# Kernel tuning notes

Measured on AMD Instinct MI355X. Metric: run time of the kernel, lower is better.

The kernel has to match this reference:

```python
import jax, jax.numpy as jnp
import numpy as np
from jax import lax

N = 2048


def setup_inputs() -> dict:
    key = jax.random.key(0)
    k1, k2, k3, k4 = jax.random.split(key, 4)
    root_logits = jax.random.normal(k1, (N,), jnp.float32)
    e = jax.random.normal(k2, (N, N), jnp.float32)
    # torch init zeros the diagonal of edge_probs
    edge_logits = e * (1.0 - jnp.eye(N, dtype=jnp.float32))
    # Gumbel noise made explicit so the reference is deterministic
    g_root = jax.random.gumbel(k3, (2, N), jnp.float32)
    g_edge = jax.random.gumbel(k4, (N, 2, N), jnp.float32)
    return {"root_logits": root_logits, "edge_logits": edge_logits,
            "g_root": g_root, "g_edge": g_edge}


def _sample_dag(root_logits, edge_logits, g_root, g_edge):
    n = root_logits.shape[0]
    f32 = jnp.float32
    i32 = jnp.int32

    # --- root sampling: hard gumbel-softmax over {root, not-root}, tau=1 ---
    yr = jnp.stack([jax.nn.log_sigmoid(root_logits),
                    jax.nn.log_sigmoid(-root_logits)]) + g_root  # [2, n]
    soft_r = jax.nn.softmax(yr, axis=0)[0]
    root_bool = yr[0] > yr[1]
    # straight-through: hard forward, soft gradient
    roots = root_bool.astype(f32) + soft_r - lax.stop_gradient(soft_r)

    # --- per-node edge sampling (noise pre-drawn; rows masked by BFS) ---
    ye = jnp.stack([jax.nn.log_sigmoid(edge_logits),
                    jax.nn.log_sigmoid(-edge_logits)], axis=1) + g_edge  # [n,2,n]
    soft_e = jax.nn.softmax(ye, axis=1)[:, 0, :]  # [n, n]
    hard_e = ye[:, 0, :] > ye[:, 1, :]            # [n, n] bool
    st_e = hard_e.astype(f32) + soft_e - lax.stop_gradient(soft_e)

    # --- FIFO queue init with roots in ascending index order ---
    idx = jnp.arange(n, dtype=i32)
    rank = jnp.cumsum(root_bool.astype(i32)) - 1
    pos = jnp.where(root_bool, rank, n)  # slot n is a write-only dump
    queue0 = jnp.zeros(n + 1, i32).at[pos].set(idx, mode='drop')
    tail0 = jnp.sum(root_bool).astype(i32)
    head0 = jnp.int32(0)
    dag0 = jnp.zeros((n, n), f32)
    anc0 = jnp.eye(n, dtype=bool)  # ancestors, anc[i,i]=1
    enq0 = root_bool               # dedup flag (equivalent to torch's pop-skip)

    def step(carry, _):
        dag, anc, queue, enq, head, tail = carry
        active = head < tail
        i = queue[head]
        anc_i = anc[i]  # includes i itself (eye init)
        cand = (1.0 - anc_i.astype(f32)) * (1.0 - roots)
        row = st_e[i] * cand
        dag = dag.at[i].set(jnp.where(active, row, dag[i]))
        children = hard_e[i] & (~anc_i) & (~root_bool) & active
        # anc[j] |= anc[i] | {i} for each child j (anc_i already contains i)
        anc = anc | (children[:, None] & anc_i[None, :])
        new = children & (~enq)
        r = jnp.cumsum(new.astype(i32)) - 1
        p = jnp.where(new, tail + r, n)
        queue = queue.at[p].set(idx, mode='drop')
        enq = enq | new
        tail = tail + jnp.sum(new).astype(i32)
        head = head + active.astype(i32)
        return (dag, anc, queue, enq, head, tail), None

    (dag, _, _, _, _, _), _ = lax.scan(
        step, (dag0, anc0, queue0, enq0, head0, tail0), None, length=n)
    return dag


def reference(root_logits, edge_logits, g_root, g_edge):
    return _sample_dag(root_logits, edge_logits, g_root, g_edge)
```

## Files before the change

kernel.cpp:

```cpp
#include <hip/hip_runtime.h>
#include <stdint.h>

typedef unsigned long long u64;
typedef unsigned int u32;
typedef unsigned short u16;

#define NN 2048
#define NW 32

#if __has_builtin(__builtin_amdgcn_sbfe)
#define SBFE(x, o) ((u32)__builtin_amdgcn_sbfe((int)(x), (u32)(o), 1u))
#else
#define SBFE(x, o) ((u32)(-(int)(((x) >> (o)) & 1u)))
#endif

static __device__ __forceinline__ bool gumbel_gt(float x, float g0, float g1) {
    float L = log1pf(expf(-fabsf(x)));
    float a = (-(fmaxf(-x, 0.f) + L)) + g0;
    float b = (-(fmaxf( x, 0.f) + L)) + g1;
    return a > b;
}

static __device__ __forceinline__ u64 orsel2(u64 acc, u64 w0, u64 w1, u64 m, int b0) {
    u32 mm = (b0 < 32) ? (u32)m : (u32)(m >> 32);
    int sh = b0 & 31;
    u32 s0 = SBFE(mm, sh);
    u32 s1 = SBFE(mm, sh + 1);
    u32 al = (u32)acc | ((u32)w0 & s0) | ((u32)w1 & s1);
    u32 ah = (u32)(acc >> 32) | ((u32)(w0 >> 32) & s0) | ((u32)(w1 >> 32) & s1);
    return ((u64)ah << 32) | al;
}

__global__ __launch_bounds__(256) void prep_kernel(
    const float* __restrict__ edge_logits,
    const float* __restrict__ g_edge,
    u64* __restrict__ heBits)
{
    const int i    = blockIdx.x;
    const int t    = threadIdx.x;
    const int lane = t & 63;
    const int wv   = t >> 6;
    const int j0   = 512 * wv + 8 * lane;

    const float4* xe  = (const float4*)(edge_logits + (size_t)i * NN + j0);
    const float4* ge0 = (const float4*)(g_edge + (size_t)i * (2 * NN) + j0);
    const float4* ge1 = (const float4*)(g_edge + (size_t)i * (2 * NN) + NN + j0);
    float4 xa = xe[0],  xb = xe[1];
    float4 g0a = ge0[0], g0b = ge0[1];
    float4 g1a = ge1[0], g1b = ge1[1];
    float x[8]  = {xa.x, xa.y, xa.z, xa.w, xb.x, xb.y, xb.z, xb.w};
    float g0[8] = {g0a.x, g0a.y, g0a.z, g0a.w, g0b.x, g0b.y, g0b.z, g0b.w};
    float g1[8] = {g1a.x, g1a.y, g1a.z, g1a.w, g1b.x, g1b.y, g1b.z, g1b.w};

    u64 v = 0;
    #pragma unroll
    for (int e = 0; e < 8; ++e)
        v |= (u64)(gumbel_gt(x[e], g0[e], g1[e]) ? 1u : 0u) << e;
    v <<= 8 * (lane & 7);
    v |= __shfl_xor(v, 1);
    v |= __shfl_xor(v, 2);
    v |= __shfl_xor(v, 4);
    if ((lane & 7) == 0)
        heBits[(size_t)i * NW + 8 * wv + (lane >> 3)] = v;
}

static __device__ void order_body(char* smem,
    const float* __restrict__ root_logits, const float* __restrict__ g_root,
    const u64* __restrict__ heBits,
    u16* __restrict__ posr, u16* __restrict__ porderW, int* __restrict__ nrPtr)
{
    int* s_porder = (int*)smem;
    int* s_cnt    = (int*)(smem + 8192);
    u64 (*s_U)[NW]  = (u64(*)[NW])(smem + 16384);
    u64 (*s_Pg)[NW] = (u64(*)[NW])(smem + 20480);
    u16* s_pos = (u16*)(smem + 24576);
    u16* s_f   = (u16*)(smem + 28672);
    u16* s_rk  = (u16*)(smem + 32768);
    u64* s_root = (u64*)(smem + 36864);
    u64* s_enq  = (u64*)(smem + 37120);
    u64* s_F    = (u64*)(smem + 37376);
    int* s_wsum = (int*)(smem + 37632);
    int* s_woff = (int*)(smem + 37696);
    int* s_sc   = (int*)(smem + 37760);
    int &s_base = s_sc[0]; int &s_lo = s_sc[1]; int &s_levcnt = s_sc[2];
    int &s_newcnt = s_sc[3]; int &s_nr = s_sc[4];

    const int t    = threadIdx.x;
    const int lane = t & 63;
    const int wid  = t >> 6;
    const int half = lane >> 5;
    const int w    = lane & 31;

    for (int p = 0; p < 2; ++p) {
        int j = p * 1024 + t;
        bool rb = gumbel_gt(root_logits[j], g_root[j], g_root[NN + j]);
        u64 m = __ballot(rb);
        if (lane == 0) s_root[j >> 6] = m;
    }
    __syncthreads();
    for (int p = 0; p < 2; ++p) {
        int j = p * 1024 + t;
        int ww = j >> 6; u64 bit = 1ull << (j & 63);
        if (s_root[ww] & bit) {
            int r = 0;
            for (int k = 0; k < ww; ++k) r += __popcll(s_root[k]);
            r += __popcll(s_root[ww] & (bit - 1ull));
            s_pos[j] = (u16)r;
            s_porder[r] = j;
        }
    }
    if (t < NW) s_enq[t] = s_root[t];
    if (t == 0) {
        int tl = 0;
        for (int k = 0; k < NW; ++k) tl += __popcll(s_root[k]);
        s_lo = 0; s_levcnt = tl; s_base = tl; s_nr = tl;
    }
    __syncthreads();

    while (s_levcnt > 0 && s_base < NN) {
        const int lo = s_lo, cnt = s_levcnt, base = s_base;
        const int seglen = (cnt + 15) >> 4;
        const int s0 = wid * seglen;
        const int s1 = (s0 + seglen < cnt) ? (s0 + seglen) : cnt;

        {
            u64 acc = 0;
            for (int m = s0 + half; m < s1; m += 2)
                acc |= heBits[(size_t)s_porder[lo + m] * NW + w];
            acc |= __shfl(acc, lane ^ 32);
            if (half == 0) s_U[wid][w] = acc;
        }
        __syncthreads();
        if (t < NW) {
            u64 o = 0;
            #pragma unroll
            for (int s = 0; s < 16; ++s) o |= s_U[s][t];
            s_F[t] = o & ~s_enq[t] & ~s_root[t];
        }
        __syncthreads();
        if (t < 512) {
            int s = t >> 5, ww = t & 31;
            u64 p = 0;
            for (int s2 = 0; s2 < s; ++s2) p |= s_U[s2][ww];
            s_Pg[s][ww] = p & s_F[ww];
        }
        __syncthreads();
        {
            u64 P  = s_Pg[wid][w];
            u64 Fw = s_F[w];
            int myidx = (s0 + lane < s1) ? s_porder[lo + s0 + lane] : 0;
            u64 rnext = 0;
            {
                int rowi0 = __shfl(myidx, half);
                if (s0 + half < s1) rnext = heBits[(size_t)rowi0 * NW + w];
            }
            for (int m = s0; m < s1; m += 2) {
                int m0 = m + half;
                u64 r = rnext;
                {
                    int sidx = (m + 2 - s0) + half;
                    if (sidx > 63) sidx = 0;
                    int rowin = __shfl(myidx, sidx);
                    rnext = 0;
                    if (m + 2 + half < s1) rnext = heBits[(size_t)rowin * NW + w];
                }
                u64 v = (m0 < s1) ? (r & Fw & ~P) : 0ull;
                u64 vlo = __shfl(v, w);
                u64 B = half ? (v & ~vlo) : v;
                int pc = __popcll(B);
                int inc = pc;
                #pragma unroll
                for (int d = 1; d < 32; d <<= 1) {
                    int u2 = __shfl_up(inc, d, 64);
                    if (w >= d) inc += u2;
                }
                int excl = inc - pc;
                int tot = __shfl(inc, (half << 5) | 31);
                if (w == 0 && m0 < s1) s_cnt[m0] = tot;
                u64 mm = B;
                int idx = excl;
                while (mm) {
                    int b = __ffsll(mm) - 1; mm &= mm - 1;
                    int j = (w << 6) + b;
                    s_f[j]  = (u16)m0;
                    s_rk[j] = (u16)idx++;
                }
                P |= B | __shfl(B, lane ^ 32);
            }
        }
        __syncthreads();
        {
            int b0 = 2 * t, b1 = 2 * t + 1;
            int c0 = (b0 < cnt) ? s_cnt[b0] : 0;
            int c1 = (b1 < cnt) ? s_cnt[b1] : 0;
            int pairv = c0 + c1;
            int incl = pairv;
            for (int d = 1; d < 64; d <<= 1) {
                int v = __shfl_up(incl, d, 64);
                if (lane >= d) incl += v;
            }
            if (lane == 63) s_wsum[wid] = incl;
            __syncthreads();
            if (t < 16) {
                int v = s_wsum[t];
                int inc2 = v;
                for (int d = 1; d < 16; d <<= 1) {
                    int u = __shfl_up(inc2, d, 16);
                    if (t >= d) inc2 += u;
                }
                s_woff[t] = inc2 - v;
                if (t == 15) s_newcnt = inc2;
            }
            __syncthreads();
            int excl = s_woff[wid] + (incl - pairv);
            if (b0 < cnt) s_cnt[b0] = excl;
            if (b1 < cnt) s_cnt[b1] = excl + c0;
        }
        __syncthreads();
        for (int p = 0; p < 2; ++p) {
            int j = p * 1024 + t;
            int ww = j >> 6;
            if ((s_F[ww] >> (j & 63)) & 1ull) {
                int slot = base + s_cnt[s_f[j]] + s_rk[j];
                s_pos[j] = (u16)slot;
                s_porder[slot] = j;
            }
        }
        if (t < NW) s_enq[t] |= s_F[t];
        __syncthreads();
        if (t == 0) { s_lo = base; s_levcnt = s_newcnt; s_base = base + s_newcnt; }
        __syncthreads();
    }

    for (int p = 0; p < 2; ++p) {
        int j = p * 1024 + t;
        int ww = j >> 6; u64 bit = 1ull << (j & 63);
        if (!((s_enq[ww] >> (j & 63)) & 1ull)) {
            int rk = 0;
            for (int k2 = 0; k2 < ww; ++k2) rk += __popcll(~s_enq[k2]);
            rk += __popcll(~s_enq[ww] & (bit - 1ull));
            int slot = s_base + rk;
            s_pos[j] = (u16)slot;
            s_porder[slot] = j;
        }
    }
    __syncthreads();
    for (int p = 0; p < 2; ++p) {
        int j = p * 1024 + t;
        int fl = s_pos[j];
        if ((s_root[j >> 6] >> (j & 63)) & 1ull) fl |= 0x8000;
        if ((s_enq[j >> 6]  >> (j & 63)) & 1ull) fl |= 0x4000;
        posr[j] = (u16)fl;
        porderW[j] = (u16)s_porder[j];
    }
    if (t == 0) *nrPtr = s_nr;
}

__global__ __launch_bounds__(1024) void ordtrans_kernel(
    const float* __restrict__ root_logits,
    const float* __restrict__ g_root,
    const u64* __restrict__ heBits,
    u64* __restrict__ heT,
    u16* __restrict__ posr,
    u16* __restrict__ porderW,
    int* __restrict__ nrPtr)
{
    __shared__ __align__(16) char smem[38016];
    const int bid  = blockIdx.x;
    const int t    = threadIdx.x;
    const int lane = t & 63;
    const int wv   = t >> 6;

    if (bid == 0) {
        order_body(smem, root_logits, g_root, heBits, posr, porderW, nrPtr);
    } else {
        int gw = (bid - 1) * 16 + wv;
        if (gw < 1024) {
            int ti = gw >> 5, tj = gw & 31;
            u64 w = heBits[(size_t)(64 * ti + lane) * NW + tj];
            u64 out = 0;
            #pragma unroll
            for (int b = 0; b < 64; ++b) {
                u64 m = __ballot(((w >> b) & 1ull) != 0);
                if (b == lane) out = m;
            }
            heT[(size_t)(64 * tj + lane) * NW + ti] = out;
        }
    }
}

__global__ __launch_bounds__(256) void apbuild_kernel(
    const u64* __restrict__ heT, const u16* __restrict__ porderW,
    const int* __restrict__ nrPtr, u64* __restrict__ Ap)
{
    __shared__ u64 s_row[NW];
    __shared__ u16 s_inv[NN];
    __shared__ int s_invb, s_nr;
    const int b = blockIdx.x;
    const int t = threadIdx.x;
    for (int q = t; q < NN; q += 256) s_inv[q] = porderW[q];
    if (t == 0) { s_invb = porderW[b]; s_nr = *nrPtr; }
    __syncthreads();
    if (t < NW) s_row[t] = heT[(size_t)s_invb * NW + t];
    __syncthreads();
    const bool bge = (b >= s_nr);
    for (int pass = 0; pass < 8; ++pass) {
        int a = pass * 256 + t;
        int ia = s_inv[a];
        bool bit = bge && (a < b) &&
                   (((s_row[ia >> 6] >> (ia & 63)) & 1ull) != 0);
        u64 m = __ballot(bit);
        if ((t & 63) == 0) Ap[(size_t)b * NW + (a >> 6)] = m;
    }
}

__global__ __launch_bounds__(64) void diagap2_kernel(
    u64* __restrict__ Ap, u64* __restrict__ Di)
{
    const int i  = blockIdx.x;
    const int jj = blockIdx.y;
    const int j  = ((i >> 4) << 4) + jj;
    if (j > i) return;
    __shared__ u64 sm[64];
    const int r = threadIdx.x;
    u64 M = Ap[(size_t)(64 * i + r) * NW + i] | (1ull << r);
    for (int s = 0; s < 6; ++s) {
        sm[r] = M;
        __syncthreads();
        u64 acc = 0;
        #pragma unroll
        for (int b = 0; b < 64; ++b)
            acc |= sm[b] & (0ull - ((M >> b) & 1ull));
        __syncthreads();
        M = acc;
    }
    if (j == i) { Di[64 * i + r] = M; return; }
    sm[r] = Ap[(size_t)(64 * i + r) * NW + j];
    __syncthreads();
    u64 acc = 0;
    #pragma unroll
    for (int b = 0; b < 64; ++b)
        acc |= sm[b] & (0ull - ((M >> b) & 1ull));
    Ap[(size_t)(64 * i + r) * NW + j] = acc;
}

__global__ __launch_bounds__(1024) void colhalf_kernel(
    const u64* __restrict__ Ap, const u64* __restrict__ Di,
    u64* __restrict__ Anc)
{
    __shared__ __align__(16) u64 colA[16][64];
    __shared__ u64 part[16][64];
    const int t  = threadIdx.x;
    const int r  = t & 63;
    const int wv = t >> 6;
    const int k    = blockIdx.x & 15;
    const int hb   = blockIdx.x >> 4;
    const int base = hb << 4;
    const int bend = base + 16;
    const int kk   = base + k;

    for (int row = t; row < 64 * kk; row += 1024)
        Anc[(size_t)row * NW + kk] = 0ull;

    if (t < 64) {
        u64 d = Di[64 * kk + r];
        colA[0][r] = d;
        Anc[(size_t)(64 * kk + r) * NW + kk] = d;
    }
    __syncthreads();

    const int j0 = kk + wv;

    for (int ib = kk + 1; ib < bend; ib += 4) {
        u64 m0[4], acc[4];
        #pragma unroll
        for (int g = 0; g < 4; ++g) {
            int ig = ib + g;
            bool v = (ig < bend);
            m0[g] = (v && (j0 < ib)) ? Ap[(size_t)(64 * ig + r) * NW + j0] : 0ull;
            acc[g] = 0ull;
        }
        u64 tm[3][3];
        #pragma unroll
        for (int s = 0; s < 3; ++s) {
            #pragma unroll
            for (int q = 0; q < 3; ++q) {
                int g = s + 1 + q;
                tm[s][q] = (g < 4 && (ib + g) < bend)
                    ? Ap[(size_t)(64 * (ib + g) + r) * NW + (ib + s)] : 0ull;
            }
        }

        if (j0 < ib) {
            const ulonglong2* rp = (const ulonglong2*)&colA[j0 - kk][0];
            #pragma unroll
            for (int bp = 0; bp < 32; ++bp) {
                ulonglong2 ww = rp[bp];
                #pragma unroll
                for (int g = 0; g < 4; ++g)
                    acc[g] = orsel2(acc[g], ww.x, ww.y, m0[g], 2 * bp);
            }
        }

        #pragma unroll
        for (int s = 0; s < 4; ++s) {
            const int i = ib + s;
            if (i < bend) {
                part[wv][r] = acc[s];
                __syncthreads();
                if (wv < 2) {
                    u64 red = part[0][r];
                    #pragma unroll
                    for (int p = 1; p < 16; ++p) red |= part[p][r];
                    if (wv == 0) colA[i - kk][r] = red;
                    else Anc[(size_t)(64 * i + r) * NW + kk] = red;
                }
                __syncthreads();
                if (s < 3 && (i + 1) < bend) {
                    const u64* rowp = colA[i - kk];
                    #pragma unroll
                    for (int bi = 0; bi < 4; ++bi) {
                        int b = 4 * wv + bi;
                        u64 w = rowp[b];
                        u32 wl = (u32)w, wh = (u32)(w >> 32);
                        #pragma unroll
                        for (int q = 0; q < 3; ++q) {
                            int g = s + 1 + q;
                            if (g < 4) {
                                u32 sm2 = (u32)(0u - (u32)((tm[s][q] >> b) & 1ull));
                                u32 al = (u32)acc[g] | (wl & sm2);
                                u32 ah = (u32)(acc[g] >> 32) | (wh & sm2);
                                acc[g] = ((u64)ah << 32) | al;
                            }
                        }
                    }
                }
            }
        }
    }
}

__global__ __launch_bounds__(256) void merge1_kernel(
    const u64* __restrict__ Bstar,
    const u64* __restrict__ CpRows,
    u64* __restrict__ Yp)
{
    __shared__ u64 SQ[256][17];
    __shared__ u64 PL[8][4];
    const int t    = threadIdx.x;
    const int lane = t & 63;
    const int wv   = t >> 6;
    const int grp  = lane >> 4;
    const int w    = lane & 15;
    const int rb   = blockIdx.x;
    const int q    = blockIdx.y;

    if (t < 32)
        PL[t >> 2][t & 3] = Bstar[(size_t)(8 * rb + (t >> 2)) * NW + 16 + 4 * q + (t & 3)];
    for (int s = t; s < 4096; s += 256)
        SQ[s >> 4][s & 15] = CpRows[(size_t)(256 * q + (s >> 4)) * NW + (s & 15)];
    __syncthreads();

    u64 acc0 = 0, acc1 = 0;
    #pragma unroll
    for (int cw = 0; cw < 4; ++cw) {
        u64 m0 = PL[2 * wv + 0][cw];
        u64 m1 = PL[2 * wv + 1][cw];
        #pragma unroll
        for (int cc = 0; cc < 16; ++cc) {
            u64 qq = SQ[cw * 64 + cc * 4 + grp][w];
            int sh = (cc & 7) * 4 + grp;
            u32 h0 = (cc < 8) ? (u32)m0 : (u32)(m0 >> 32);
            u32 h1 = (cc < 8) ? (u32)m1 : (u32)(m1 >> 32);
            u32 ql = (u32)qq, qh = (u32)(qq >> 32);
            u32 s;
            s = SBFE(h0, sh);
            acc0 = ((u64)(((u32)(acc0 >> 32)) | (qh & s)) << 32) | (((u32)acc0) | (ql & s));
            s = SBFE(h1, sh);
            acc1 = ((u64)(((u32)(acc1 >> 32)) | (qh & s)) << 32) | (((u32)acc1) | (ql & s));
        }
    }
    acc0 |= __shfl_xor(acc0, 16); acc0 |= __shfl_xor(acc0, 32);
    acc1 |= __shfl_xor(acc1, 16); acc1 |= __shfl_xor(acc1, 32);
    if (grp == 0) {
        size_t base = ((size_t)q * 1024 + 8 * rb + 2 * wv) * 16 + w;
        Yp[base] = acc0;
        Yp[base + 16] = acc1;
    }
}

__global__ __launch_bounds__(256) void merge2_kernel(
    const u64* __restrict__ Yp,
    const u64* __restrict__ Astar,
    u64* __restrict__ Xp)
{
    __shared__ u64 SQ[256][17];
    __shared__ u64 PL[8][4];
    const int t    = threadIdx.x;
    const int lane = t & 63;
    const int wv   = t >> 6;
    const int grp  = lane >> 4;
    const int w    = lane & 15;
    const int rb   = blockIdx.x;
    const int q    = blockIdx.y;

    if (t < 32) {
        size_t idx = (size_t)(8 * rb + (t >> 2)) * 16 + 4 * q + (t & 3);
        PL[t >> 2][t & 3] = Yp[idx] | Yp[idx + 16384] | Yp[idx + 32768] | Yp[idx + 49152];
    }
    for (int s = t; s < 4096; s += 256)
        SQ[s >> 4][s & 15] = Astar[(size_t)(256 * q + (s >> 4)) * NW + (s & 15)];
    __syncthreads();

    u64 acc0 = 0, acc1 = 0;
    #pragma unroll
    for (int cw = 0; cw < 4; ++cw) {
        u64 m0 = PL[2 * wv + 0][cw];
        u64 m1 = PL[2 * wv + 1][cw];
        #pragma unroll
        for (int cc = 0; cc < 16; ++cc) {
            u64 qq = SQ[cw * 64 + cc * 4 + grp][w];
            int sh = (cc & 7) * 4 + grp;
            u32 h0 = (cc < 8) ? (u32)m0 : (u32)(m0 >> 32);
            u32 h1 = (cc < 8) ? (u32)m1 : (u32)(m1 >> 32);
            u32 ql = (u32)qq, qh = (u32)(qq >> 32);
            u32 s;
            s = SBFE(h0, sh);
            acc0 = ((u64)(((u32)(acc0 >> 32)) | (qh & s)) << 32) | (((u32)acc0) | (ql & s));
            s = SBFE(h1, sh);
            acc1 = ((u64)(((u32)(acc1 >> 32)) | (qh & s)) << 32) | (((u32)acc1) | (ql & s));
        }
    }
    acc0 |= __shfl_xor(acc0, 16); acc0 |= __shfl_xor(acc0, 32);
    acc1 |= __shfl_xor(acc1, 16); acc1 |= __shfl_xor(acc1, 32);
    if (grp == 0) {
        size_t base = ((size_t)q * 1024 + 8 * rb + 2 * wv) * 16 + w;
        Xp[base] = acc0;
        Xp[base + 16] = acc1;
    }
}

__global__ __launch_bounds__(256) void foldout_kernel(
    const u64* __restrict__ heBits,
    const u64* __restrict__ Anc,
    const u64* __restrict__ Xp,
    const u16* __restrict__ posr,
    float* __restrict__ dag)
{
    __shared__ u64 s_anc[NW];
    __shared__ u64 s_he[NW];
    __shared__ u16 s_pr[NN];
    const int i = blockIdx.x;
    const int t = threadIdx.x;

    ((int4*)s_pr)[t] = ((const int4*)posr)[t];
    __syncthreads();
    const int fl = s_pr[i];
    const int pi = fl & 0x7FF;
    if (t < NW) {
        u64 v;
        if (pi >= 1024 && t < 16) {
            size_t idx = (size_t)(pi - 1024) * 16 + t;
            v = Xp[idx] | Xp[idx + 16384] | Xp[idx + 32768] | Xp[idx + 49152];
        } else {
            v = Anc[(size_t)pi * NW + t];
        }
        s_anc[t] = v;
        s_he[t]  = heBits[(size_t)i * NW + t];
    }
    __syncthreads();
    const bool reach_i = (fl & 0x4000) != 0;
    const int j0 = t * 8;
    float o[8];
    #pragma unroll
    for (int e = 0; e < 8; ++e) {
        int j = j0 + e;
        int pr = s_pr[j];
        int a = pr & 0x7FF;
        bool he = ((s_he[j >> 6] >> (j & 63)) & 1ull) != 0;
        bool anc = ((s_anc[a >> 6] >> (a & 63)) & 1ull) != 0;
        o[e] = (reach_i && he && ((pr & 0x8000) == 0) && !anc) ? 1.f : 0.f;
    }
    float4* outp = (float4*)(dag + (size_t)i * NN + j0);
    outp[0] = make_float4(o[0], o[1], o[2], o[3]);
    outp[1] = make_float4(o[4], o[5], o[6], o[7]);
}

extern "C" void kernel_launch(void* const* d_in, const int* in_sizes, int n_in,
                              void* d_out, int out_size, void* d_ws, size_t ws_size,
                              hipStream_t stream) {
    const float* root_logits = (const float*)d_in[0];
    const float* edge_logits = (const float*)d_in[1];
    const float* g_root      = (const float*)d_in[2];
    const float* g_edge      = (const float*)d_in[3];
    float* dag = (float*)d_out;

    char* ws = (char*)d_ws;
    u64* heBits  = (u64*)(ws);
    u64* heT     = (u64*)(ws + (512 << 10));
    u64* Ap      = (u64*)(ws + (1 << 20));
    u64* Anc     = (u64*)(ws + (1 << 20) + (512 << 10));
    u64* Di      = (u64*)(ws + (2 << 20));
    u16* posr    = (u16*)(ws + (2 << 20) + (192 << 10));
    u16* porderW = (u16*)(ws + (2 << 20) + (196 << 10));
    int* nrPtr   = (int*)(ws + (2 << 20) + (200 << 10));
    u64* Yp      = (u64*)(ws + (3 << 20));
    u64* Xp      = (u64*)(ws + (3 << 20) + (512 << 10));

    prep_kernel    <<<NN, 256, 0, stream>>>(edge_logits, g_edge, heBits);
    ordtrans_kernel<<<256, 1024, 0, stream>>>(root_logits, g_root, heBits, heT,
                                              posr, porderW, nrPtr);
    apbuild_kernel <<<NN, 256, 0, stream>>>(heT, porderW, nrPtr, Ap);
    diagap2_kernel <<<dim3(NW, 16), 64, 0, stream>>>(Ap, Di);
    colhalf_kernel <<<NW, 1024, 0, stream>>>(Ap, Di, Anc);
    merge1_kernel  <<<dim3(128, 4), 256, 0, stream>>>(Anc + (size_t)1024 * NW,
                                                      Ap + (size_t)1024 * NW, Yp);
    merge2_kernel  <<<dim3(128, 4), 256, 0, stream>>>(Yp, Anc, Xp);
    foldout_kernel <<<NN, 256, 0, stream>>>(heBits, Anc, Xp, posr, dag);
}
```

Measured before the change: 127.6 us.

## Fuse diagonal closure into column kernel using wave shuffles

Removes the separate diagap2 kernel. The 64x64 diagonal-block transitive closure is now computed inside colhalf_kernel: each wave computes the closure of one diagonal block with __shfl instead of shared memory and barriers. The off-diagonal left-multiplication by the closure, which diagap2 used to write back into Ap, now happens after the reduction step. Anc is written once at the end from colA. This saves a launch and a global round trip, at the cost of redundant diagonal closures in every block and extra shuffle work on the serial critical path.

New measurement: 178.7 us. 40.1% more time.

```diff
diff --git a/kernel.cpp b/kernel.cpp
--- a/kernel.cpp
+++ b/kernel.cpp
@@ -314,42 +314,12 @@
     }
 }
 
-__global__ __launch_bounds__(64) void diagap2_kernel(
-    u64* __restrict__ Ap, u64* __restrict__ Di)
-{
-    const int i  = blockIdx.x;
-    const int jj = blockIdx.y;
-    const int j  = ((i >> 4) << 4) + jj;
-    if (j > i) return;
-    __shared__ u64 sm[64];
-    const int r = threadIdx.x;
-    u64 M = Ap[(size_t)(64 * i + r) * NW + i] | (1ull << r);
-    for (int s = 0; s < 6; ++s) {
-        sm[r] = M;
-        __syncthreads();
-        u64 acc = 0;
-        #pragma unroll
-        for (int b = 0; b < 64; ++b)
-            acc |= sm[b] & (0ull - ((M >> b) & 1ull));
-        __syncthreads();
-        M = acc;
-    }
-    if (j == i) { Di[64 * i + r] = M; return; }
-    sm[r] = Ap[(size_t)(64 * i + r) * NW + j];
-    __syncthreads();
-    u64 acc = 0;
-    #pragma unroll
-    for (int b = 0; b < 64; ++b)
-        acc |= sm[b] & (0ull - ((M >> b) & 1ull));
-    Ap[(size_t)(64 * i + r) * NW + j] = acc;
-}
-
 __global__ __launch_bounds__(1024) void colhalf_kernel(
-    const u64* __restrict__ Ap, const u64* __restrict__ Di,
-    u64* __restrict__ Anc)
+    const u64* __restrict__ Ap, u64* __restrict__ Anc)
 {
     __shared__ __align__(16) u64 colA[16][64];
     __shared__ u64 part[16][64];
+    __shared__ u64 s_di[16][64];
     const int t  = threadIdx.x;
     const int r  = t & 63;
     const int wv = t >> 6;
@@ -362,11 +332,21 @@
     for (int row = t; row < 64 * kk; row += 1024)
         Anc[(size_t)row * NW + kk] = 0ull;
 
-    if (t < 64) {
-        u64 d = Di[64 * kk + r];
-        colA[0][r] = d;
-        Anc[(size_t)(64 * kk + r) * NW + kk] = d;
-    }
+    {
+        const int I = base + wv;
+        u64 M = Ap[(size_t)(64 * I + r) * NW + I] | (1ull << r);
+        for (int s = 0; s < 6; ++s) {
+            u64 acc = 0;
+            #pragma unroll 8
+            for (int b = 0; b < 64; ++b)
+                acc |= __shfl(M, b) & (0ull - ((M >> b) & 1ull));
+            M = acc;
+        }
+        s_di[wv][r] = M;
+    }
+    __syncthreads();
+
+    if (t < 64) colA[0][r] = s_di[k][r];
     __syncthreads();
 
     const int j0 = kk + wv;
@@ -408,12 +388,16 @@
             if (i < bend) {
                 part[wv][r] = acc[s];
                 __syncthreads();
-                if (wv < 2) {
+                if (wv == 0) {
                     u64 red = part[0][r];
                     #pragma unroll
                     for (int p = 1; p < 16; ++p) red |= part[p][r];
-                    if (wv == 0) colA[i - kk][r] = red;
-                    else Anc[(size_t)(64 * i + r) * NW + kk] = red;
+                    u64 d = s_di[i - base][r];
+                    u64 out = 0;
+                    #pragma unroll 8
+                    for (int b = 0; b < 64; ++b)
+                        out |= __shfl(red, b) & (0ull - ((d >> b) & 1ull));
+                    colA[i - kk][r] = out;
                 }
                 __syncthreads();
                 if (s < 3 && (i + 1) < bend) {
@@ -438,6 +422,13 @@
             }
         }
     }
+
+    {
+        int m = t >> 6;
+        int rr = t & 63;
+        if (kk + m < bend)
+            Anc[(size_t)(64 * (kk + m) + rr) * NW + kk] = colA[m][rr];
+    }
 }
 
 __global__ __launch_bounds__(256) void merge1_kernel(
@@ -600,7 +591,6 @@
     u64* heT     = (u64*)(ws + (512 << 10));
     u64* Ap      = (u64*)(ws + (1 << 20));
     u64* Anc     = (u64*)(ws + (1 << 20) + (512 << 10));
-    u64* Di      = (u64*)(ws + (2 << 20));
     u16* posr    = (u16*)(ws + (2 << 20) + (192 << 10));
     u16* porderW = (u16*)(ws + (2 << 20) + (196 << 10));
     int* nrPtr   = (int*)(ws + (2 << 20) + (200 << 10));
@@ -611,8 +601,7 @@
     ordtrans_kernel<<<256, 1024, 0, stream>>>(root_logits, g_root, heBits, heT,
                                               posr, porderW, nrPtr);
     apbuild_kernel <<<NN, 256, 0, stream>>>(heT, porderW, nrPtr, Ap);
-    diagap2_kernel <<<dim3(NW, 16), 64, 0, stream>>>(Ap, Di);
-    colhalf_kernel <<<NW, 1024, 0, stream>>>(Ap, Di, Anc);
+    colhalf_kernel <<<NW, 1024, 0, stream>>>(Ap, Anc);
     merge1_kernel  <<<dim3(128, 4), 256, 0, stream>>>(Anc + (size_t)1024 * NW,
                                                       Ap + (size_t)1024 * NW, Yp);
     merge2_kernel  <<<dim3(128, 4), 256, 0, stream>>>(Yp, Anc, Xp);
```
